# Optimization experiments

Measured on AMD Instinct MI355X. Metric: run time of the kernel, lower is better.

Reference implementation:

```python
import jax, jax.numpy as jnp
import numpy as np

N, E, ND, ED, H, OUT, L, VC = 10000, 160000, 8, 4, 128, 256, 6, 6
HEADS, C = 4, 128  # GATConv: out_channels=128 per head, concat=False -> mean over heads


def _ln(x, g, b, eps=1e-5):
    m = x.mean(-1, keepdims=True)
    v = ((x - m) ** 2).mean(-1, keepdims=True)
    return (x - m) * jax.lax.rsqrt(v + eps) * g + b


def _gat_layer(h, src, dst, e_attr, lw, a_src, a_dst, lew, a_edge, bias):
    # h: [N,H]; e_attr: [Etot,H]; PyG GATConv(heads=4, concat=False, edge_dim=H)
    xh = (h @ lw).reshape(N, HEADS, C)                 # [N,4,128]
    eh = (e_attr @ lew).reshape(-1, HEADS, C)          # [Etot,4,128]
    al_s = jnp.einsum('nhc,hc->nh', xh, a_src)
    al_d = jnp.einsum('nhc,hc->nh', xh, a_dst)
    al_e = jnp.einsum('ehc,hc->eh', eh, a_edge)
    alpha = jax.nn.leaky_relu(al_s[src] + al_d[dst] + al_e, 0.2)  # [Etot,4]
    amax = jax.ops.segment_max(alpha, dst, num_segments=N)
    ex = jnp.exp(alpha - amax[dst])
    den = jax.ops.segment_sum(ex, dst, num_segments=N)
    w = ex / (den[dst] + 1e-16)
    out = jax.ops.segment_sum(xh[src] * w[..., None], dst, num_segments=N)  # [N,4,128]
    return out.mean(axis=1) + bias


def setup_inputs() -> dict:
    key = jax.random.key(0)
    ks = jax.random.split(key, 32)
    s = 0.05
    d = {
        'x': jax.random.normal(ks[0], (N, ND), jnp.float32),
        'edge_index': jax.random.randint(ks[1], (2, E), 0, N),
        'edge_attr': jax.random.uniform(ks[2], (E, ED), jnp.float32),
        'vnf_context': jax.random.normal(ks[3], (1, VC), jnp.float32),
        # node embedding
        'node_w': jax.random.normal(ks[4], (ND, H)) * s, 'node_b': jnp.zeros((H,)),
        # EdgeAttentionLayer
        'ea_proj_w': jax.random.normal(ks[5], (ED, H)) * s, 'ea_proj_b': jnp.zeros((H,)),
        'vnf_w': jax.random.normal(ks[6], (VC, H)) * s, 'vnf_b': jnp.zeros((H,)),
        'att1_w': jax.random.normal(ks[7], (2 * H, H)) * s, 'att1_b': jnp.zeros((H,)),
        'att2_w': jax.random.normal(ks[8], (H, H // 2)) * s, 'att2_b': jnp.zeros((H // 2,)),
        'att3_w': jax.random.normal(ks[9], (H // 2, 1)) * s, 'att3_b': jnp.zeros((1,)),
        # per-layer GATConv params (stacked over L layers)
        'gat_lin_w': jax.random.normal(ks[10], (L, H, HEADS * C)) * s,
        'gat_att_src': jax.random.normal(ks[11], (L, HEADS, C)) * s,
        'gat_att_dst': jax.random.normal(ks[12], (L, HEADS, C)) * s,
        'gat_lin_edge_w': jax.random.normal(ks[13], (L, H, HEADS * C)) * s,
        'gat_att_edge': jax.random.normal(ks[14], (L, HEADS, C)) * s,
        'gat_bias': jnp.zeros((L, C)),
        'ln_scale': jnp.ones((L, H)), 'ln_bias': jnp.zeros((L, H)),
        # output projection
        'out_w': jax.random.normal(ks[15], (H, OUT)) * s, 'out_b': jnp.zeros((OUT,)),
    }
    return d


def reference(x, edge_index, edge_attr, vnf_context, node_w, node_b, ea_proj_w, ea_proj_b,
              vnf_w, vnf_b, att1_w, att1_b, att2_w, att2_b, att3_w, att3_b,
              gat_lin_w, gat_att_src, gat_att_dst, gat_lin_edge_w, gat_att_edge, gat_bias,
              ln_scale, ln_bias, out_w, out_b):
    src, dst = edge_index[0], edge_index[1]
    h = x @ node_w + node_b                                   # [N,128]
    # EdgeAttentionLayer (eval mode, no network_state)
    ef = edge_attr @ ea_proj_w + ea_proj_b                    # [E,128]
    vnf = vnf_context @ vnf_w + vnf_b                         # [1,128]
    comb = jnp.concatenate([ef, jnp.broadcast_to(vnf, (E, H))], axis=-1)
    a = jax.nn.relu(comb @ att1_w + att1_b)
    a = jax.nn.relu(a @ att2_w + att2_b)
    e_gate = jax.nn.sigmoid(a @ att3_w + att3_b)              # [E,1]
    w_edge = ef * e_gate                                      # [E,128]
    # GATConv default add_self_loops=True, fill_value='mean'
    loop = jnp.arange(N)
    src2 = jnp.concatenate([src, loop])
    dst2 = jnp.concatenate([dst, loop])
    e2 = jnp.concatenate([w_edge, jnp.broadcast_to(w_edge.mean(0, keepdims=True), (N, H))], axis=0)
    for l in range(L):
        hc = _gat_layer(h, src2, dst2, e2, gat_lin_w[l], gat_att_src[l], gat_att_dst[l],
                        gat_lin_edge_w[l], gat_att_edge[l], gat_bias[l])
        h = _ln(h + jax.nn.relu(hc), ln_scale[l], ln_bias[l])
    return h @ out_w + out_b                                  # [N,256]
```

## Files before the change

### kernel.cpp

```cpp
#include <hip/hip_runtime.h>
#include <hip/hip_bf16.h>
#include <math.h>

#define Nn 10000
#define Ee 160000
#define ET 170000
#define LL 6

typedef short v8s __attribute__((ext_vector_type(8)));
typedef float v4f __attribute__((ext_vector_type(4)));
typedef float v2f __attribute__((ext_vector_type(2)));

__device__ __forceinline__ unsigned short f2bf(float v) {
    unsigned int b = __float_as_uint(v);
    b += 0x7fffu + ((b >> 16) & 1u);
    return (unsigned short)(b >> 16);
}
__device__ __forceinline__ float bflo(unsigned int u) { return __uint_as_float(u << 16); }
__device__ __forceinline__ float bfhi(unsigned int u) { return __uint_as_float(u & 0xffff0000u); }

__global__ void k_node_embed(const float* __restrict__ x, const float* __restrict__ nw,
                             const float* __restrict__ nb, float* __restrict__ h,
                             unsigned short* __restrict__ hb) {
    int idx = blockIdx.x * 256 + threadIdx.x;
    if (idx >= Nn * 128) return;
    int n = idx >> 7, c = idx & 127;
    const float* xr = x + (size_t)n * 8;
    float acc = nb[c];
#pragma unroll
    for (int k = 0; k < 8; k++) acc += xr[k] * nw[k * 128 + c];
    h[idx] = acc;
    hb[idx] = f2bf(acc);
}

__global__ void k_small(const float* __restrict__ vnfc, const float* __restrict__ vw,
                        const float* __restrict__ vb, const float* __restrict__ eab,
                        const float* __restrict__ a1w, const float* __restrict__ a1b,
                        const float* __restrict__ eaw, float* __restrict__ E1) {
    __shared__ float vr[128];
    __shared__ float sM1[512];
    __shared__ float sd1[128];
    int t = threadIdx.x;
    if (t < 128) {
        float a = vb[t];
#pragma unroll
        for (int k = 0; k < 6; k++) a += vnfc[k] * vw[k * 128 + t];
        vr[t] = a;
    }
    __syncthreads();
    if (t < 128) {
        float a = a1b[t];
        for (int k = 0; k < 128; k++) a += eab[k] * a1w[k * 128 + t];
        for (int k = 0; k < 128; k++) a += vr[k] * a1w[(128 + k) * 128 + t];
        sd1[t] = a;
    }
    {
        int r = t >> 7, j = t & 127;
        float a = 0.f;
        for (int k = 0; k < 128; k++) a += eaw[r * 128 + k] * a1w[k * 128 + j];
        sM1[r * 128 + j] = a;
    }
    __syncthreads();
    if (t < 128) {
        E1[t * 8 + 0] = sM1[t];
        E1[t * 8 + 1] = sM1[128 + t];
        E1[t * 8 + 2] = sM1[256 + t];
        E1[t * 8 + 3] = sM1[384 + t];
        E1[t * 8 + 4] = sd1[t];
        E1[t * 8 + 5] = 0.f; E1[t * 8 + 6] = 0.f; E1[t * 8 + 7] = 0.f;
    }
}

__global__ void k_bmat(const float* __restrict__ glw, const float* __restrict__ gas,
                       const float* __restrict__ gad, const float* __restrict__ glew,
                       const float* __restrict__ gae, float* __restrict__ Bs,
                       float* __restrict__ Bd, float* __restrict__ Be) {
    int idx = blockIdx.x * 256 + threadIdx.x;
    if (idx >= LL * 128 * 4) return;
    int hh = idx & 3, k = (idx >> 2) & 127, l = idx >> 9;
    const float* lwp = glw  + (size_t)l * 65536 + k * 512 + hh * 128;
    const float* lep = glew + (size_t)l * 65536 + k * 512 + hh * 128;
    const float* sp = gas + l * 512 + hh * 128;
    const float* dp = gad + l * 512 + hh * 128;
    const float* ep = gae + l * 512 + hh * 128;
    float s1 = 0, s2 = 0, s3 = 0;
    for (int c = 0; c < 128; c++) {
        float lv = lwp[c];
        s1 += lv * sp[c];
        s2 += lv * dp[c];
        s3 += lep[c] * ep[c];
    }
    Bs[idx] = s1; Bd[idx] = s2; Be[idx] = s3;
}

__global__ void k_wsum(const float* __restrict__ glw, unsigned short* __restrict__ WsumT) {
    int idx = blockIdx.x * 256 + threadIdx.x;
    if (idx >= LL * 128 * 512) return;
    int kk = idx & 511;
    int c = (idx >> 9) & 127;
    int l = idx >> 16;
    float v = 0.25f * glw[(size_t)l * 65536 + (size_t)(kk & 127) * 512 + (kk >> 7) * 128 + c];
    WsumT[(size_t)l * 65536 + (size_t)c * 512 + kk] = f2bf(v);
}

__global__ void k_pb(const float* __restrict__ eaw, const float* __restrict__ eab,
                     const float* __restrict__ Be, float* __restrict__ PB,
                     float* __restrict__ cB) {
    int t = threadIdx.x;
    if (t >= 24) return;
    int l = t >> 2, hh = t & 3;
    const float* bp = Be + l * 512 + hh;
    float s0 = 0, s1 = 0, s2 = 0, s3 = 0, sc = 0;
    for (int k = 0; k < 128; k++) {
        float bv = bp[k * 4];
        s0 += eaw[0 * 128 + k] * bv;
        s1 += eaw[1 * 128 + k] * bv;
        s2 += eaw[2 * 128 + k] * bv;
        s3 += eaw[3 * 128 + k] * bv;
        sc += eab[k] * bv;
    }
    PB[0 * 24 + t] = s0; PB[1 * 24 + t] = s1;
    PB[2 * 24 + t] = s2; PB[3 * 24 + t] = s3;
    cB[t] = sc;
}

__global__ __launch_bounds__(256, 3) void k_edge(
    const float* __restrict__ ea, const float* __restrict__ E1,
    const float* __restrict__ a2w, const float* __restrict__ a2b,
    const float* __restrict__ a3w, const float* __restrict__ a3b,
    float* __restrict__ Gg, float4* __restrict__ Ge4, float* __restrict__ gsum) {
    __shared__ float sw2[128 * 64];
    __shared__ float4 sM[128];
    __shared__ float sD[128];
    __shared__ float prs[4][256];
    __shared__ float gsh[256];
    int t = threadIdx.x;
    int lane = t & 63;
    int p = t >> 6;
    int ps = __builtin_amdgcn_readfirstlane(p);
    for (int z = t; z < 2048; z += 256) ((float4*)sw2)[z] = ((const float4*)a2w)[z];
    if (t < 128) { sM[t] = *(const float4*)(E1 + t * 8); sD[t] = E1[t * 8 + 4]; }
    __syncthreads();
    int eb = blockIdx.x * 256 + lane;
    float4 ev[4];
#pragma unroll
    for (int r = 0; r < 4; r++) ev[r] = *(const float4*)(ea + (size_t)(eb + r * 64) * 4);
    v2f acc[4][8];
#pragma unroll
    for (int j = 0; j < 8; j++) {
        v2f b = {a2b[ps * 16 + 2 * j], a2b[ps * 16 + 2 * j + 1]};
#pragma unroll
        for (int r = 0; r < 4; r++) acc[r][j] = b;
    }
    const float* w2base = sw2 + ps * 16;
    for (int k = 0; k < 128; k++) {
        float4 m = sM[k];
        float dk = sD[k];
        v2f xx[4];
#pragma unroll
        for (int r = 0; r < 4; r++) {
            float xv = fmaxf(dk + ev[r].x * m.x + ev[r].y * m.y + ev[r].z * m.z + ev[r].w * m.w, 0.f);
            xx[r][0] = xv; xx[r][1] = xv;
        }
        const float* w2r = w2base + k * 64;
#pragma unroll
        for (int j4 = 0; j4 < 4; j4++) {
            float4 wv = *(const float4*)(w2r + j4 * 4);
            v2f w01 = {wv.x, wv.y}, w23 = {wv.z, wv.w};
#pragma unroll
            for (int r = 0; r < 4; r++) {
                acc[r][2 * j4]     += xx[r] * w01;
                acc[r][2 * j4 + 1] += xx[r] * w23;
            }
        }
    }
#pragma unroll
    for (int r = 0; r < 4; r++) {
        float pr = 0.f;
#pragma unroll
        for (int j = 0; j < 8; j++) {
            pr += fmaxf(acc[r][j][0], 0.f) * a3w[ps * 16 + 2 * j];
            pr += fmaxf(acc[r][j][1], 0.f) * a3w[ps * 16 + 2 * j + 1];
        }
        prs[p][r * 64 + lane] = pr;
    }
    __syncthreads();
    if (p == 0) {
        float v0 = 0.f, v1 = 0.f, v2 = 0.f, v3 = 0.f, v4 = 0.f;
#pragma unroll
        for (int rep = 0; rep < 4; rep++) {
            int le = rep * 64 + lane;
            float tot = prs[0][le] + prs[1][le] + prs[2][le] + prs[3][le] + a3b[0];
            float g = 1.f / (1.f + __expf(-tot));
            gsh[le] = g;
            float4 evv = ev[rep];
            v0 += g; v1 += g * evv.x; v2 += g * evv.y; v3 += g * evv.z; v4 += g * evv.w;
        }
#pragma unroll
        for (int d = 32; d > 0; d >>= 1) {
            v0 += __shfl_down(v0, d); v1 += __shfl_down(v1, d); v2 += __shfl_down(v2, d);
            v3 += __shfl_down(v3, d); v4 += __shfl_down(v4, d);
        }
        if (lane == 0) {
            atomicAdd(&gsum[0], v0); atomicAdd(&gsum[1], v1); atomicAdd(&gsum[2], v2);
            atomicAdd(&gsum[3], v3); atomicAdd(&gsum[4], v4);
        }
    }
    __syncthreads();
    {
        int e = blockIdx.x * 256 + ps * 64 + lane;
        float g = gsh[ps * 64 + lane];
        float4 evv = *(const float4*)(ea + (size_t)e * 4);
        Gg[e] = g;
        Ge4[e] = make_float4(g * evv.x, g * evv.y, g * evv.z, g * evv.w);
    }
}

__global__ void k_hist(const int* __restrict__ ei, int* __restrict__ hist) {
    int i = blockIdx.x * 256 + threadIdx.x;
    if (i >= ET) return;
    int d = (i < Ee) ? ei[Ee + i] : (i - Ee);
    atomicAdd(&hist[d], 1);
}

__global__ __launch_bounds__(1024) void k_scan(const int* __restrict__ hist,
                                               int* __restrict__ seg, int* __restrict__ pos) {
    __shared__ int wsums[16];
    __shared__ int carry_s;
    int t = threadIdx.x;
    int lane = t & 63, wid = t >> 6;
    if (t == 0) { carry_s = 0; seg[0] = 0; }
    __syncthreads();
    for (int base = 0; base < Nn; base += 1024) {
        int idx = base + t;
        int v = (idx < Nn) ? hist[idx] : 0;
        int sc = v;
#pragma unroll
        for (int d = 1; d < 64; d <<= 1) {
            int up = __shfl_up(sc, d);
            if (lane >= d) sc += up;
        }
        if (lane == 63) wsums[wid] = sc;
        __syncthreads();
        if (wid == 0) {
            int wv = (lane < 16) ? wsums[lane] : 0;
            int wsc = wv;
#pragma unroll
            for (int d = 1; d < 16; d <<= 1) {
                int up = __shfl_up(wsc, d);
                if (lane >= d) wsc += up;
            }
            if (lane < 16) wsums[lane] = wsc - wv;
        }
        __syncthreads();
        int carry = carry_s;
        int inc = sc + wsums[wid] + carry;
        if (idx < Nn) { seg[idx + 1] = inc; pos[idx] = inc - v; }
        __syncthreads();
        if (t == 1023) carry_s = inc;
        __syncthreads();
    }
}

__global__ void k_scatter(const int* __restrict__ ei, int* __restrict__ pos,
                          int2* __restrict__ pse) {
    int i = blockIdx.x * 256 + threadIdx.x;
    if (i >= ET) return;
    int s, d;
    if (i < Ee) { s = ei[i]; d = ei[Ee + i]; } else { s = d = i - Ee; }
    int idx = atomicAdd(&pos[d], 1);
    pse[idx] = make_int2(s, i);
}

__global__ void k_gperm(const int2* __restrict__ pse, const float* __restrict__ Gg,
                        const float4* __restrict__ Ge4, const float* __restrict__ gsum,
                        float* __restrict__ Gsg, float4* __restrict__ Gse) {
    int i = blockIdx.x * 256 + threadIdx.x;
    if (i >= ET) return;
    int y = pse[i].y;
    if (y < Ee) {
        Gsg[i] = Gg[y];
        Gse[i] = Ge4[y];
    } else {
        float inv = 1.f / Ee;
        Gsg[i] = gsum[0] * inv;
        Gse[i] = make_float4(gsum[1] * inv, gsum[2] * inv, gsum[3] * inv, gsum[4] * inv);
    }
}

__global__ void k_ab(const float* __restrict__ h, const float* __restrict__ Bs_l,
                     const float* __restrict__ Bd_l, float* __restrict__ als,
                     float* __restrict__ ald) {
    int idx = blockIdx.x * 256 + threadIdx.x;
    if (idx >= Nn * 8) return;
    int n = idx >> 3, slot = idx & 7;
    const float* B = (slot < 4) ? Bs_l : Bd_l;
    int hh = slot & 3;
    const float4* hr = (const float4*)(h + (size_t)n * 128);
    float s = 0.f;
#pragma unroll 8
    for (int kb = 0; kb < 32; kb++) {
        float4 hv = hr[kb];
        s += hv.x * B[(4 * kb + 0) * 4 + hh] + hv.y * B[(4 * kb + 1) * 4 + hh]
           + hv.z * B[(4 * kb + 2) * 4 + hh] + hv.w * B[(4 * kb + 3) * 4 + hh];
    }
    if (slot < 4) als[n * 4 + hh] = s;
    else          ald[n * 4 + hh] = s;
}

__global__ __launch_bounds__(256) void k_agg3(
    const int2* __restrict__ pse, const int* __restrict__ seg,
    const float* __restrict__ als, const float* __restrict__ ald,
    const float* __restrict__ Gsg, const float4* __restrict__ Gse,
    const float* __restrict__ PB, const float* __restrict__ cB, int l,
    const unsigned short* __restrict__ hb, unsigned short* __restrict__ aggb) {
    __shared__ float part[2][512];
    __shared__ float pden[2][4];
    int t = threadIdx.x;
    int lane = t & 63;
    int wv = (t >> 6) & 1;
    int w = t >> 7;
    int n = blockIdx.x * 2 + w;
    int start = seg[n], end = seg[n + 1];
    int deg = end - start;
    int half = (deg + 1) >> 1;
    int s0 = start + wv * half;
    int e0 = wv ? end : start + half;
    int hp = lane >> 4;
    int cch = (lane & 15) * 8;
    float aldh = ald[n * 4 + hp];
    float c0 = cB[l * 4 + hp];
    float pc0 = PB[0 * 24 + l * 4 + hp];
    float pc1 = PB[1 * 24 + l * 4 + hp];
    float pc2 = PB[2 * 24 + l * 4 + hp];
    float pc3 = PB[3 * 24 + l * 4 + hp];
    float den = 0.f;
    float4 acc0 = make_float4(0.f, 0.f, 0.f, 0.f);
    float4 acc1 = make_float4(0.f, 0.f, 0.f, 0.f);
    int i = s0;
    for (; i + 2 <= e0; i += 2) {
        int sa = pse[i].x, sb = pse[i + 1].x;
        float ga = Gsg[i], gbv = Gsg[i + 1];
        float4 ga4 = Gse[i], gb4 = Gse[i + 1];
        float ala = ga * c0 + ga4.x * pc0 + ga4.y * pc1 + ga4.z * pc2 + ga4.w * pc3;
        float alb = gbv * c0 + gb4.x * pc0 + gb4.y * pc1 + gb4.z * pc2 + gb4.w * pc3;
        float ava = als[sa * 4 + hp] + aldh + ala;
        float avb = als[sb * 4 + hp] + aldh + alb;
        ava = ava > 0.f ? ava : 0.2f * ava;
        avb = avb > 0.f ? avb : 0.2f * avb;
        float ea = __expf(fminf(ava, 60.f));
        float eb = __expf(fminf(avb, 60.f));
        den += ea + eb;
        uint4 ua = *(const uint4*)(hb + (size_t)sa * 128 + cch);
        uint4 ub = *(const uint4*)(hb + (size_t)sb * 128 + cch);
        acc0.x += ea * bflo(ua.x) + eb * bflo(ub.x);
        acc0.y += ea * bfhi(ua.x) + eb * bfhi(ub.x);
        acc0.z += ea * bflo(ua.y) + eb * bflo(ub.y);
        acc0.w += ea * bfhi(ua.y) + eb * bfhi(ub.y);
        acc1.x += ea * bflo(ua.z) + eb * bflo(ub.z);
        acc1.y += ea * bfhi(ua.z) + eb * bfhi(ub.z);
        acc1.z += ea * bflo(ua.w) + eb * bflo(ub.w);
        acc1.w += ea * bfhi(ua.w) + eb * bfhi(ub.w);
    }
    if (i < e0) {
        int sa = pse[i].x;
        float ga = Gsg[i];
        float4 ga4 = Gse[i];
        float ala = ga * c0 + ga4.x * pc0 + ga4.y * pc1 + ga4.z * pc2 + ga4.w * pc3;
        float ava = als[sa * 4 + hp] + aldh + ala;
        ava = ava > 0.f ? ava : 0.2f * ava;
        float ea = __expf(fminf(ava, 60.f));
        den += ea;
        uint4 ua = *(const uint4*)(hb + (size_t)sa * 128 + cch);
        acc0.x += ea * bflo(ua.x); acc0.y += ea * bfhi(ua.x);
        acc0.z += ea * bflo(ua.y); acc0.w += ea * bfhi(ua.y);
        acc1.x += ea * bflo(ua.z); acc1.y += ea * bfhi(ua.z);
        acc1.z += ea * bflo(ua.w); acc1.w += ea * bfhi(ua.w);
    }
    if (wv == 1) {
        *(float4*)&part[w][lane * 8] = acc0;
        *(float4*)&part[w][lane * 8 + 4] = acc1;
        if ((lane & 15) == 0) pden[w][hp] = den;
    }
    __syncthreads();
    if (wv == 0) {
        float4 p0 = *(const float4*)&part[w][lane * 8];
        float4 p1 = *(const float4*)&part[w][lane * 8 + 4];
        float inv = 1.f / (den + pden[w][hp] + 1e-16f);
        acc0.x = (acc0.x + p0.x) * inv; acc0.y = (acc0.y + p0.y) * inv;
        acc0.z = (acc0.z + p0.z) * inv; acc0.w = (acc0.w + p0.w) * inv;
        acc1.x = (acc1.x + p1.x) * inv; acc1.y = (acc1.y + p1.y) * inv;
        acc1.z = (acc1.z + p1.z) * inv; acc1.w = (acc1.w + p1.w) * inv;
        ushort4 q0, q1;
        q0.x = f2bf(acc0.x); q0.y = f2bf(acc0.y); q0.z = f2bf(acc0.z); q0.w = f2bf(acc0.w);
        q1.x = f2bf(acc1.x); q1.y = f2bf(acc1.y); q1.z = f2bf(acc1.z); q1.w = f2bf(acc1.w);
        *(ushort4*)(aggb + (size_t)n * 512 + lane * 8) = q0;
        *(ushort4*)(aggb + (size_t)n * 512 + lane * 8 + 4) = q1;
    }
}

__global__ __launch_bounds__(256) void k_post(
    const unsigned short* __restrict__ aggb, const unsigned short* __restrict__ WsumT_l,
    const float* __restrict__ gbias, const float* __restrict__ lnsc,
    const float* __restrict__ lnbi, float* __restrict__ h,
    unsigned short* __restrict__ hb, const float* __restrict__ Bs_n,
    const float* __restrict__ Bd_n, float* __restrict__ als, float* __restrict__ ald) {
    int t = threadIdx.x;
    int lane = t & 63, w = t >> 6;
    int n0 = (blockIdx.x * 4 + w) * 16;
    if (n0 >= Nn) return;
    int m = lane & 15, q = lane >> 4;
    v4f acc[8];
#pragma unroll
    for (int nt = 0; nt < 8; nt++) acc[nt] = (v4f){0.f, 0.f, 0.f, 0.f};
    const unsigned short* arow = aggb + (size_t)(n0 + m) * 512 + q * 8;
#pragma unroll 4
    for (int ks = 0; ks < 16; ks++) {
        v8s fa = *(const v8s*)(arow + ks * 32);
#pragma unroll
        for (int nt = 0; nt < 8; nt++) {
            int col = nt * 16 + m;
            v8s fb = *(const v8s*)(WsumT_l + (size_t)col * 512 + ks * 32 + q * 8);
            acc[nt] = __builtin_amdgcn_mfma_f32_16x16x32_bf16(fa, fb, acc[nt], 0, 0, 0);
        }
    }
    float v[8][4];
    float s1[4] = {0.f, 0.f, 0.f, 0.f}, s2[4] = {0.f, 0.f, 0.f, 0.f};
#pragma unroll
    for (int nt = 0; nt < 8; nt++) {
        int col = nt * 16 + m;
        float b = gbias[col];
#pragma unroll
        for (int r = 0; r < 4; r++) {
            int row = n0 + q * 4 + r;
            float val = h[(size_t)row * 128 + col] + fmaxf(acc[nt][r] + b, 0.f);
            v[nt][r] = val;
            s1[r] += val; s2[r] += val * val;
        }
    }
#pragma unroll
    for (int d = 1; d <= 8; d <<= 1) {
#pragma unroll
        for (int r = 0; r < 4; r++) {
            s1[r] += __shfl_xor(s1[r], d);
            s2[r] += __shfl_xor(s2[r], d);
        }
    }
    float o8[8][4];
#pragma unroll
    for (int r = 0; r < 4; r++) {
        float mean = s1[r] * (1.f / 128.f);
        float var = s2[r] * (1.f / 128.f) - mean * mean;
        float rinv = rsqrtf(var + 1e-5f);
        int row = n0 + q * 4 + r;
#pragma unroll
        for (int nt = 0; nt < 8; nt++) {
            int col = nt * 16 + m;
            float o = (v[nt][r] - mean) * rinv * lnsc[col] + lnbi[col];
            o8[nt][r] = o;
            h[(size_t)row * 128 + col] = o;
            hb[(size_t)row * 128 + col] = f2bf(o);
        }
    }
    float sal[4][4], sad[4][4];
#pragma unroll
    for (int r = 0; r < 4; r++) {
#pragma unroll
        for (int hh = 0; hh < 4; hh++) { sal[r][hh] = 0.f; sad[r][hh] = 0.f; }
    }
#pragma unroll
    for (int nt = 0; nt < 8; nt++) {
        int col = nt * 16 + m;
        float4 bs = *(const float4*)(Bs_n + col * 4);
        float4 bd = *(const float4*)(Bd_n + col * 4);
#pragma unroll
        for (int r = 0; r < 4; r++) {
            float o = o8[nt][r];
            sal[r][0] += o * bs.x; sal[r][1] += o * bs.y;
            sal[r][2] += o * bs.z; sal[r][3] += o * bs.w;
            sad[r][0] += o * bd.x; sad[r][1] += o * bd.y;
            sad[r][2] += o * bd.z; sad[r][3] += o * bd.w;
        }
    }
#pragma unroll
    for (int d = 1; d <= 8; d <<= 1) {
#pragma unroll
        for (int r = 0; r < 4; r++) {
#pragma unroll
            for (int hh = 0; hh < 4; hh++) {
                sal[r][hh] += __shfl_xor(sal[r][hh], d);
                sad[r][hh] += __shfl_xor(sad[r][hh], d);
            }
        }
    }
    if (m < 8) {
        int hh = m & 3;
#pragma unroll
        for (int r = 0; r < 4; r++) {
            int row = n0 + q * 4 + r;
            float va = (hh == 0) ? sal[r][0] : (hh == 1) ? sal[r][1] : (hh == 2) ? sal[r][2] : sal[r][3];
            float vd = (hh == 0) ? sad[r][0] : (hh == 1) ? sad[r][1] : (hh == 2) ? sad[r][2] : sad[r][3];
            if (m < 4) als[row * 4 + hh] = va;
            else       ald[row * 4 + hh] = vd;
        }
    }
}

__global__ __launch_bounds__(256) void k_out(
    const float* __restrict__ h, const float* __restrict__ ow,
    const float* __restrict__ ob, float* __restrict__ out) {
    __shared__ float4 hs4[8][32];
    int t = threadIdx.x;
    int n0 = blockIdx.x * 8;
    if (t < 256) {
        int i = t >> 5, kb = t & 31;
        hs4[i][kb] = *(const float4*)(h + (size_t)(n0 + i) * 128 + 4 * kb);
    }
    __syncthreads();
    float acc[8] = {0, 0, 0, 0, 0, 0, 0, 0};
    for (int kb = 0; kb < 32; kb++) {
        float w0 = ow[(4 * kb + 0) * 256 + t];
        float w1 = ow[(4 * kb + 1) * 256 + t];
        float w2 = ow[(4 * kb + 2) * 256 + t];
        float w3 = ow[(4 * kb + 3) * 256 + t];
#pragma unroll
        for (int i = 0; i < 8; i++) {
            float4 hv = hs4[i][kb];
            acc[i] += hv.x * w0 + hv.y * w1 + hv.z * w2 + hv.w * w3;
        }
    }
    float b = ob[t];
#pragma unroll
    for (int i = 0; i < 8; i++) out[(size_t)(n0 + i) * 256 + t] = acc[i] + b;
}

extern "C" void kernel_launch(void* const* d_in, const int* in_sizes, int n_in,
                              void* d_out, int out_size, void* d_ws, size_t ws_size,
                              hipStream_t stream) {
    const float* x    = (const float*)d_in[0];
    const int*   ei   = (const int*)d_in[1];
    const float* ea   = (const float*)d_in[2];
    const float* vnfc = (const float*)d_in[3];
    const float* nw   = (const float*)d_in[4];
    const float* nb   = (const float*)d_in[5];
    const float* eaw  = (const float*)d_in[6];
    const float* eab  = (const float*)d_in[7];
    const float* vw   = (const float*)d_in[8];
    const float* vb   = (const float*)d_in[9];
    const float* a1w  = (const float*)d_in[10];
    const float* a1b  = (const float*)d_in[11];
    const float* a2w  = (const float*)d_in[12];
    const float* a2b  = (const float*)d_in[13];
    const float* a3w  = (const float*)d_in[14];
    const float* a3b  = (const float*)d_in[15];
    const float* glw  = (const float*)d_in[16];
    const float* gas  = (const float*)d_in[17];
    const float* gad  = (const float*)d_in[18];
    const float* glew = (const float*)d_in[19];
    const float* gae  = (const float*)d_in[20];
    const float* gb   = (const float*)d_in[21];
    const float* lnsc = (const float*)d_in[22];
    const float* lnbi = (const float*)d_in[23];
    const float* ow   = (const float*)d_in[24];
    const float* ob   = (const float*)d_in[25];
    float* out = (float*)d_out;

    char* w = (char*)d_ws;
    size_t o = 0;
    auto allocf = [&](size_t cnt) { float* p = (float*)(w + o); o += ((cnt * 4 + 255) / 256) * 256; return p; };
    auto alloci = [&](size_t cnt) { int* p = (int*)(w + o); o += ((cnt * 4 + 255) / 256) * 256; return p; };
    auto allocu = [&](size_t cnt) { unsigned short* p = (unsigned short*)(w + o); o += ((cnt * 2 + 255) / 256) * 256; return p; };
    float* h      = allocf((size_t)Nn * 128);
    unsigned short* hb    = allocu((size_t)Nn * 128);
    unsigned short* aggb  = allocu((size_t)Nn * 512);
    unsigned short* WsumT = allocu((size_t)LL * 128 * 512);
    float* als    = allocf((size_t)Nn * 4);
    float* ald    = allocf((size_t)Nn * 4);
    float* Gg     = allocf((size_t)Ee);
    float4* Ge4   = (float4*)allocf((size_t)Ee * 4);
    float* Gsg    = allocf((size_t)ET);
    float4* Gse   = (float4*)allocf((size_t)ET * 4);
    float* Bs     = allocf(3072);
    float* Bd     = allocf(3072);
    float* Be     = allocf(3072);
    float* E1     = allocf(1024);
    float* PB     = allocf(96);
    float* cB     = allocf(24);
    float* gsum   = allocf(8);
    int* seg  = alloci(Nn + 1);
    int* hist = alloci(Nn);
    int* pos  = alloci(Nn);
    int2* pse = (int2*)alloci((size_t)ET * 2);

    hipMemsetAsync(hist, 0, Nn * sizeof(int), stream);
    hipMemsetAsync(gsum, 0, 8 * sizeof(float), stream);

    k_node_embed<<<(Nn * 128 + 255) / 256, 256, 0, stream>>>(x, nw, nb, h, hb);
    k_small<<<1, 512, 0, stream>>>(vnfc, vw, vb, eab, a1w, a1b, eaw, E1);
    k_bmat<<<(LL * 128 * 4 + 255) / 256, 256, 0, stream>>>(glw, gas, gad, glew, gae, Bs, Bd, Be);
    k_wsum<<<(LL * 128 * 512 + 255) / 256, 256, 0, stream>>>(glw, WsumT);
    k_pb<<<1, 32, 0, stream>>>(eaw, eab, Be, PB, cB);
    k_edge<<<Ee / 256, 256, 0, stream>>>(ea, E1, a2w, a2b, a3w, a3b, Gg, Ge4, gsum);
    k_hist<<<(ET + 255) / 256, 256, 0, stream>>>(ei, hist);
    k_scan<<<1, 1024, 0, stream>>>(hist, seg, pos);
    k_scatter<<<(ET + 255) / 256, 256, 0, stream>>>(ei, pos, pse);
    k_gperm<<<(ET + 255) / 256, 256, 0, stream>>>(pse, Gg, Ge4, gsum, Gsg, Gse);
    k_ab<<<(Nn * 8 + 255) / 256, 256, 0, stream>>>(h, Bs, Bd, als, ald);
    for (int l = 0; l < LL; l++) {
        int ln = (l + 1) % LL;
        k_agg3<<<Nn / 2, 256, 0, stream>>>(pse, seg, als, ald, Gsg, Gse, PB, cB, l, hb, aggb);
        k_post<<<(625 + 3) / 4, 256, 0, stream>>>(aggb, WsumT + (size_t)l * 65536,
                                                  gb + l * 128, lnsc + l * 128, lnbi + l * 128,
                                                  h, hb, Bs + ln * 512, Bd + ln * 512, als, ald);
    }
    k_out<<<Nn / 8, 256, 0, stream>>>(h, ow, ob, out);
}
```

Before: 574.5 us.

## Precompute per-layer edge attention logits once and split aggregation across four waves

Edge attention terms for all six layers are now computed once in a preprocessing kernel and stored as float4 per edge per layer. The per-layer aggregation loop then loads one float4 instead of a scalar plus a float4 and five FMAs. Aggregation also moves from two nodes per block with two waves each to one node per block split across four waves, reducing in shared memory. The cost is a larger precomputed buffer (6×170k×16 bytes) and more blocks with less work per wave, since mean degree is about 17.

```diff
diff --git a/kernel.cpp b/kernel.cpp
--- a/kernel.cpp
+++ b/kernel.cpp
@@ -272,19 +272,33 @@
     pse[idx] = make_int2(s, i);
 }
 
-__global__ void k_gperm(const int2* __restrict__ pse, const float* __restrict__ Gg,
-                        const float4* __restrict__ Ge4, const float* __restrict__ gsum,
-                        float* __restrict__ Gsg, float4* __restrict__ Gse) {
+__global__ void k_ales(const int2* __restrict__ pse, const float* __restrict__ Gg,
+                       const float4* __restrict__ Ge4, const float* __restrict__ gsum,
+                       const float* __restrict__ PB, const float* __restrict__ cB,
+                       float4* __restrict__ aleS) {
     int i = blockIdx.x * 256 + threadIdx.x;
     if (i >= ET) return;
     int y = pse[i].y;
-    if (y < Ee) {
-        Gsg[i] = Gg[y];
-        Gse[i] = Ge4[y];
-    } else {
+    float g;
+    float4 ge;
+    if (y < Ee) { g = Gg[y]; ge = Ge4[y]; }
+    else {
         float inv = 1.f / Ee;
-        Gsg[i] = gsum[0] * inv;
-        Gse[i] = make_float4(gsum[1] * inv, gsum[2] * inv, gsum[3] * inv, gsum[4] * inv);
+        g = gsum[0] * inv;
+        ge = make_float4(gsum[1] * inv, gsum[2] * inv, gsum[3] * inv, gsum[4] * inv);
+    }
+#pragma unroll
+    for (int l = 0; l < LL; l++) {
+        float4 o;
+        o.x = g * cB[l * 4 + 0] + ge.x * PB[0 * 24 + l * 4 + 0] + ge.y * PB[1 * 24 + l * 4 + 0]
+            + ge.z * PB[2 * 24 + l * 4 + 0] + ge.w * PB[3 * 24 + l * 4 + 0];
+        o.y = g * cB[l * 4 + 1] + ge.x * PB[0 * 24 + l * 4 + 1] + ge.y * PB[1 * 24 + l * 4 + 1]
+            + ge.z * PB[2 * 24 + l * 4 + 1] + ge.w * PB[3 * 24 + l * 4 + 1];
+        o.z = g * cB[l * 4 + 2] + ge.x * PB[0 * 24 + l * 4 + 2] + ge.y * PB[1 * 24 + l * 4 + 2]
+            + ge.z * PB[2 * 24 + l * 4 + 2] + ge.w * PB[3 * 24 + l * 4 + 2];
+        o.w = g * cB[l * 4 + 3] + ge.x * PB[0 * 24 + l * 4 + 3] + ge.y * PB[1 * 24 + l * 4 + 3]
+            + ge.z * PB[2 * 24 + l * 4 + 3] + ge.w * PB[3 * 24 + l * 4 + 3];
+        aleS[(size_t)l * ET + i] = o;
     }
 }
 
@@ -308,42 +322,34 @@
     else          ald[n * 4 + hh] = s;
 }
 
-__global__ __launch_bounds__(256) void k_agg3(
+__global__ __launch_bounds__(256) void k_agg4(
     const int2* __restrict__ pse, const int* __restrict__ seg,
     const float* __restrict__ als, const float* __restrict__ ald,
-    const float* __restrict__ Gsg, const float4* __restrict__ Gse,
-    const float* __restrict__ PB, const float* __restrict__ cB, int l,
-    const unsigned short* __restrict__ hb, unsigned short* __restrict__ aggb) {
-    __shared__ float part[2][512];
-    __shared__ float pden[2][4];
+    const float4* __restrict__ aleS_l, const unsigned short* __restrict__ hb,
+    unsigned short* __restrict__ aggb) {
+    __shared__ float part[3][512];
+    __shared__ float pden[3][4];
     int t = threadIdx.x;
     int lane = t & 63;
-    int wv = (t >> 6) & 1;
-    int w = t >> 7;
-    int n = blockIdx.x * 2 + w;
+    int wv = t >> 6;
+    int n = blockIdx.x;
     int start = seg[n], end = seg[n + 1];
     int deg = end - start;
-    int half = (deg + 1) >> 1;
-    int s0 = start + wv * half;
-    int e0 = wv ? end : start + half;
+    int quarter = (deg + 3) >> 2;
+    int s0 = start + wv * quarter;
+    int e0 = min(s0 + quarter, end);
     int hp = lane >> 4;
     int cch = (lane & 15) * 8;
     float aldh = ald[n * 4 + hp];
-    float c0 = cB[l * 4 + hp];
-    float pc0 = PB[0 * 24 + l * 4 + hp];
-    float pc1 = PB[1 * 24 + l * 4 + hp];
-    float pc2 = PB[2 * 24 + l * 4 + hp];
-    float pc3 = PB[3 * 24 + l * 4 + hp];
     float den = 0.f;
     float4 acc0 = make_float4(0.f, 0.f, 0.f, 0.f);
     float4 acc1 = make_float4(0.f, 0.f, 0.f, 0.f);
     int i = s0;
     for (; i + 2 <= e0; i += 2) {
         int sa = pse[i].x, sb = pse[i + 1].x;
-        float ga = Gsg[i], gbv = Gsg[i + 1];
-        float4 ga4 = Gse[i], gb4 = Gse[i + 1];
-        float ala = ga * c0 + ga4.x * pc0 + ga4.y * pc1 + ga4.z * pc2 + ga4.w * pc3;
-        float alb = gbv * c0 + gb4.x * pc0 + gb4.y * pc1 + gb4.z * pc2 + gb4.w * pc3;
+        float4 ala4 = aleS_l[i], alb4 = aleS_l[i + 1];
+        float ala = hp == 0 ? ala4.x : hp == 1 ? ala4.y : hp == 2 ? ala4.z : ala4.w;
+        float alb = hp == 0 ? alb4.x : hp == 1 ? alb4.y : hp == 2 ? alb4.z : alb4.w;
         float ava = als[sa * 4 + hp] + aldh + ala;
         float avb = als[sb * 4 + hp] + aldh + alb;
         ava = ava > 0.f ? ava : 0.2f * ava;
@@ -364,9 +370,8 @@
     }
     if (i < e0) {
         int sa = pse[i].x;
-        float ga = Gsg[i];
-        float4 ga4 = Gse[i];
-        float ala = ga * c0 + ga4.x * pc0 + ga4.y * pc1 + ga4.z * pc2 + ga4.w * pc3;
+        float4 ala4 = aleS_l[i];
+        float ala = hp == 0 ? ala4.x : hp == 1 ? ala4.y : hp == 2 ? ala4.z : ala4.w;
         float ava = als[sa * 4 + hp] + aldh + ala;
         ava = ava > 0.f ? ava : 0.2f * ava;
         float ea = __expf(fminf(ava, 60.f));
@@ -377,20 +382,24 @@
         acc1.x += ea * bflo(ua.z); acc1.y += ea * bfhi(ua.z);
         acc1.z += ea * bflo(ua.w); acc1.w += ea * bfhi(ua.w);
     }
-    if (wv == 1) {
-        *(float4*)&part[w][lane * 8] = acc0;
-        *(float4*)&part[w][lane * 8 + 4] = acc1;
-        if ((lane & 15) == 0) pden[w][hp] = den;
+    if (wv > 0) {
+        *(float4*)&part[wv - 1][lane * 8] = acc0;
+        *(float4*)&part[wv - 1][lane * 8 + 4] = acc1;
+        if ((lane & 15) == 0) pden[wv - 1][hp] = den;
     }
     __syncthreads();
     if (wv == 0) {
-        float4 p0 = *(const float4*)&part[w][lane * 8];
-        float4 p1 = *(const float4*)&part[w][lane * 8 + 4];
-        float inv = 1.f / (den + pden[w][hp] + 1e-16f);
-        acc0.x = (acc0.x + p0.x) * inv; acc0.y = (acc0.y + p0.y) * inv;
-        acc0.z = (acc0.z + p0.z) * inv; acc0.w = (acc0.w + p0.w) * inv;
-        acc1.x = (acc1.x + p1.x) * inv; acc1.y = (acc1.y + p1.y) * inv;
-        acc1.z = (acc1.z + p1.z) * inv; acc1.w = (acc1.w + p1.w) * inv;
+        float dtot = den + pden[0][hp] + pden[1][hp] + pden[2][hp];
+#pragma unroll
+        for (int r = 0; r < 3; r++) {
+            float4 p0 = *(const float4*)&part[r][lane * 8];
+            float4 p1 = *(const float4*)&part[r][lane * 8 + 4];
+            acc0.x += p0.x; acc0.y += p0.y; acc0.z += p0.z; acc0.w += p0.w;
+            acc1.x += p1.x; acc1.y += p1.y; acc1.z += p1.z; acc1.w += p1.w;
+        }
+        float inv = 1.f / (dtot + 1e-16f);
+        acc0.x *= inv; acc0.y *= inv; acc0.z *= inv; acc0.w *= inv;
+        acc1.x *= inv; acc1.y *= inv; acc1.z *= inv; acc1.w *= inv;
         ushort4 q0, q1;
         q0.x = f2bf(acc0.x); q0.y = f2bf(acc0.y); q0.z = f2bf(acc0.z); q0.w = f2bf(acc0.w);
         q1.x = f2bf(acc1.x); q1.y = f2bf(acc1.y); q1.z = f2bf(acc1.z); q1.w = f2bf(acc1.w);
@@ -578,8 +587,7 @@
     float* ald    = allocf((size_t)Nn * 4);
     float* Gg     = allocf((size_t)Ee);
     float4* Ge4   = (float4*)allocf((size_t)Ee * 4);
-    float* Gsg    = allocf((size_t)ET);
-    float4* Gse   = (float4*)allocf((size_t)ET * 4);
+    float4* aleS  = (float4*)allocf((size_t)LL * ET * 4);
     float* Bs     = allocf(3072);
     float* Bd     = allocf(3072);
     float* Be     = allocf(3072);
@@ -604,11 +612,11 @@
     k_hist<<<(ET + 255) / 256, 256, 0, stream>>>(ei, hist);
     k_scan<<<1, 1024, 0, stream>>>(hist, seg, pos);
     k_scatter<<<(ET + 255) / 256, 256, 0, stream>>>(ei, pos, pse);
-    k_gperm<<<(ET + 255) / 256, 256, 0, stream>>>(pse, Gg, Ge4, gsum, Gsg, Gse);
+    k_ales<<<(ET + 255) / 256, 256, 0, stream>>>(pse, Gg, Ge4, gsum, PB, cB, aleS);
     k_ab<<<(Nn * 8 + 255) / 256, 256, 0, stream>>>(h, Bs, Bd, als, ald);
     for (int l = 0; l < LL; l++) {
         int ln = (l + 1) % LL;
-        k_agg3<<<Nn / 2, 256, 0, stream>>>(pse, seg, als, ald, Gsg, Gse, PB, cB, l, hb, aggb);
+        k_agg4<<<Nn, 256, 0, stream>>>(pse, seg, als, ald, aleS + (size_t)l * ET, hb, aggb);
         k_post<<<(625 + 3) / 4, 256, 0, stream>>>(aggb, WsumT + (size_t)l * 65536,
                                                   gb + l * 128, lnsc + l * 128, lnbi + l * 128,
                                                   h, hb, Bs + ln * 512, Bd + ln * 512, als, ald);
```

After: 564.2 us. No clear change (-1.8%).
